# Kernel tuning notes

Measured on AMD Instinct MI355X. Metric: run time of the kernel, lower is better.

## Reference

```python
import jax, jax.numpy as jnp
import numpy as np

K_DIM, V_DIM, D_K, D_V, N_HEAD = 1024, 1024, 64, 64, 16


def setup_inputs() -> dict:
    key = jax.random.key(0)
    ks = jax.random.split(key, 7)
    B, LQ, LK = 2, 2048, 2048
    q = jax.random.normal(ks[0], (B, LQ, K_DIM), dtype=jnp.float32)
    k = jax.random.normal(ks[1], (B, LK, K_DIM), dtype=jnp.float32)
    v = jax.random.normal(ks[2], (B, LK, V_DIM), dtype=jnp.float32)
    s = 0.02
    w_q = jax.random.normal(ks[3], (N_HEAD * D_K, K_DIM), dtype=jnp.float32) * s
    w_k = jax.random.normal(ks[4], (N_HEAD * D_K, K_DIM), dtype=jnp.float32) * s
    w_v = jax.random.normal(ks[5], (N_HEAD * D_V, V_DIM), dtype=jnp.float32) * s
    fc_y = jax.random.normal(ks[6], (V_DIM, N_HEAD * D_V), dtype=jnp.float32) * s
    return {"q": q, "k": k, "v": v, "w_q": w_q, "w_k": w_k, "w_v": w_v, "fc_y": fc_y}


def reference(q, k, v, w_q, w_k, w_v, fc_y):
    B, LQ, _ = q.shape
    LK = k.shape[1]
    # projections: Linear(x) = x @ W.T, then split heads -> (b, h, l, d)
    qh = (q @ w_q.T).reshape(B, LQ, N_HEAD, D_K).transpose(0, 2, 1, 3)
    kh = (k @ w_k.T).reshape(B, LK, N_HEAD, D_K).transpose(0, 2, 1, 3)
    vh = (v @ w_v.T).reshape(B, LK, N_HEAD, D_V).transpose(0, 2, 1, 3)
    # NOTE: original ScaledDotProductAttention uses k.size(2), which for
    # 4D (b, h, len_k, d_k) inputs is len_k, NOT d_k. Replicate faithfully.
    scale = kh.shape[2] ** 0.5  # == sqrt(len_k)
    scores = jnp.einsum('bhqd,bhkd->bhqk', qh, kh) / scale
    attn = jax.nn.softmax(scores, axis=-1)  # (b, h, lq, lk)
    yh = jnp.einsum('bhqk,bhkd->bhqd', attn, vh)
    y = yh.transpose(0, 2, 1, 3).reshape(B, LQ, N_HEAD * D_V)
    y = y @ fc_y.T  # (b, lq, v_dim)
    return (y, attn)
```

## Files before the change

### kernel.cpp

```cpp
#include <hip/hip_runtime.h>

typedef __attribute__((ext_vector_type(8))) short short8;
typedef __attribute__((ext_vector_type(4))) short short4v;
typedef __attribute__((ext_vector_type(4))) float f32x4;

__device__ __forceinline__ short f2bf(float f) {
  unsigned u = __float_as_uint(f);
  u += 0x7fff + ((u >> 16) & 1);
  return (short)(u >> 16);
}

__device__ __forceinline__ void async16(const short* g, short* l) {
  __builtin_amdgcn_global_load_lds(
      (__attribute__((address_space(1))) unsigned int*)(g),
      (__attribute__((address_space(3))) unsigned int*)(l), 16, 0, 0);
}

__global__ __launch_bounds__(256) void cvt_w(const float* __restrict__ w0, const float* __restrict__ w1,
                                             const float* __restrict__ w2, const float* __restrict__ w3,
                                             short* __restrict__ o0, short* __restrict__ o1,
                                             short* __restrict__ o2, short* __restrict__ o3) {
  const int bid = blockIdx.x;
  const int seg = bid >> 9;
  const float* s = seg == 0 ? w0 : seg == 1 ? w1 : seg == 2 ? w2 : w3;
  short* d = seg == 0 ? o0 : seg == 1 ? o1 : seg == 2 ? o2 : o3;
  const int idx = ((bid & 511) * 256 + (int)threadIdx.x) * 8;
  float4 x = *(const float4*)(s + idx);
  float4 y = *(const float4*)(s + idx + 4);
  short8 t;
  t[0] = f2bf(x.x); t[1] = f2bf(x.y); t[2] = f2bf(x.z); t[3] = f2bf(x.w);
  t[4] = f2bf(y.x); t[5] = f2bf(y.y); t[6] = f2bf(y.z); t[7] = f2bf(y.w);
  *(short8*)(d + idx) = t;
}

__device__ __forceinline__ void ldf32(const float* src, int K, int kt, int tid, f32x4* r) {
  const int row = tid >> 4, c = (tid & 15) * 4;
  const float* p = src + (long)row * K + kt + c;
#pragma unroll
  for (int j = 0; j < 8; j++) r[j] = *(const f32x4*)(p + (long)(j * 16) * K);
}
__device__ __forceinline__ void wrf32(short* dst, int stride, int tid, const f32x4* r) {
  const int row = tid >> 4, c = (tid & 15) * 4;
#pragma unroll
  for (int j = 0; j < 8; j++) {
    short4v t;
    t[0] = f2bf(r[j][0]); t[1] = f2bf(r[j][1]); t[2] = f2bf(r[j][2]); t[3] = f2bf(r[j][3]);
    *(short4v*)&dst[(row + j * 16) * stride + c] = t;
  }
}
__device__ __forceinline__ void ldbf16(const short* src, int K, int kt, int tid, short* lds) {
  const int w = tid >> 6, l = tid & 63;
#pragma unroll
  for (int i = 0; i < 4; i++) {
    const int seg = i * 4 + w;
    const int o = seg * 1024 + l * 16;
    const int row = o >> 7, col = (o & 127) >> 1;
    async16(src + (long)row * K + kt + col, lds + seg * 512);
  }
}

template <int AF32, int BF32, int MODE>
__device__ __forceinline__ void gemm_core(const void* Ap, const void* Bp, void* Cout,
                                          int bm, int bn, int bz, int N, int K, int tid,
                                          short* As, short* Bs) {
  constexpr int SA = AF32 ? 72 : 64;
  constexpr int SB = BF32 ? 72 : 64;
  const int wave = tid >> 6, lane = tid & 63, quad = lane >> 4, l16 = lane & 15;
  const int wm = (wave >> 1) * 64, wn = (wave & 1) * 64;
  const float* A32 = (const float*)Ap + (long)bm * 128 * K;
  const short* A16 = (const short*)Ap + (long)bm * 128 * K;
  const float* B32 = (const float*)Bp + (long)bn * 128 * K;
  const short* B16 = (const short*)Bp + (long)bn * 128 * K;

  const f32x4 zero = {0.f, 0.f, 0.f, 0.f};
  f32x4 acc[4][4];
#pragma unroll
  for (int i = 0; i < 4; i++)
#pragma unroll
    for (int j = 0; j < 4; j++) acc[i][j] = zero;

  f32x4 ar[8], br[8];
  if (AF32) { ldf32(A32, K, 0, tid, ar); wrf32(As, SA, tid, ar); }
  else ldbf16(A16, K, 0, tid, As);
  if (BF32) { ldf32(B32, K, 0, tid, br); wrf32(Bs, SB, tid, br); }
  else ldbf16(B16, K, 0, tid, Bs);
  __syncthreads();

  const int NT = K >> 6;
  int cur = 0;
  for (int t = 0; t < NT; ++t) {
    short* Ac = As + cur * 128 * SA;
    short* Bc = Bs + cur * 128 * SB;
    short* An = As + (cur ^ 1) * 128 * SA;
    short* Bn = Bs + (cur ^ 1) * 128 * SB;
    const bool more = (t + 1 < NT);
    if (more) {
      if (AF32) ldf32(A32, K, (t + 1) * 64, tid, ar);
      else ldbf16(A16, K, (t + 1) * 64, tid, An);
      if (BF32) ldf32(B32, K, (t + 1) * 64, tid, br);
      else ldbf16(B16, K, (t + 1) * 64, tid, Bn);
    }
#pragma unroll
    for (int kk = 0; kk < 64; kk += 32) {
      short8 af[4], bf[4];
#pragma unroll
      for (int i = 0; i < 4; i++) af[i] = *(const short8*)&Ac[(wm + i * 16 + l16) * SA + kk + quad * 8];
#pragma unroll
      for (int j = 0; j < 4; j++) bf[j] = *(const short8*)&Bc[(wn + j * 16 + l16) * SB + kk + quad * 8];
#pragma unroll
      for (int i = 0; i < 4; i++)
#pragma unroll
        for (int j = 0; j < 4; j++)
          acc[i][j] = __builtin_amdgcn_mfma_f32_16x16x32_bf16(af[i], bf[j], acc[i][j], 0, 0, 0);
    }
    if (more) {
      if (AF32) wrf32(An, SA, tid, ar);
      if (BF32) wrf32(Bn, SB, tid, br);
    }
    __syncthreads();
    cur ^= 1;
  }

#pragma unroll
  for (int i = 0; i < 4; i++)
#pragma unroll
    for (int j = 0; j < 4; j++)
#pragma unroll
      for (int r = 0; r < 4; r++) {
        const int grow = bm * 128 + wm + i * 16 + quad * 4 + r;
        const int gcol = bn * 128 + wn + j * 16 + l16;
        const float val = acc[i][j][r];
        if (MODE == 0) {
          const int b = grow >> 11, l = grow & 2047, hh = gcol >> 6, d = gcol & 63;
          ((short*)Cout)[((long)(b * 16 + hh) * 2048 + l) * 64 + d] = f2bf(val);
        } else if (MODE == 1) {
          ((short*)Cout)[((long)bz * 1024 + grow) * 2048 + gcol] = f2bf(val);
        } else {
          ((float*)Cout)[(long)grow * N + gcol] = val;
        }
      }
}

__global__ __launch_bounds__(256) void proj_fused(const float* __restrict__ q, const float* __restrict__ k,
                                                  const float* __restrict__ v,
                                                  const short* __restrict__ wqb, const short* __restrict__ wkb,
                                                  const short* __restrict__ wvb,
                                                  short* __restrict__ qh, short* __restrict__ kh,
                                                  short* __restrict__ vht) {
  __shared__ __align__(16) short As[2 * 128 * 72];
  __shared__ __align__(16) short Bs[2 * 128 * 72];
  const int p = blockIdx.x, tid = threadIdx.x;
  const int id = (p & 7) * 96 + (p >> 3);
  if (id < 512) {
    const int seg = id >> 8, t = id & 255;
    const int bm = t >> 3, bn = t & 7;
    gemm_core<1, 0, 0>(seg ? (const void*)k : (const void*)q,
                       seg ? (const void*)wkb : (const void*)wqb,
                       seg ? (void*)kh : (void*)qh,
                       bm, bn, 0, 1024, 1024, tid, As, Bs);
  } else {
    const int lid = id - 512;
    const int bz = lid >> 7, t = lid & 127;
    gemm_core<0, 1, 1>(wvb, v + (long)bz * 2048 * 1024, vht,
                       t & 7, t >> 3, bz, 2048, 1024, tid, As, Bs);
  }
}

__global__ __launch_bounds__(256) void gemm_final(const short* __restrict__ yhb, const short* __restrict__ fcb,
                                                  float* __restrict__ y) {
  __shared__ __align__(16) short As[2 * 128 * 72];
  __shared__ __align__(16) short Bs[2 * 128 * 72];
  const int p = blockIdx.x;
  const int id = (p & 7) * 32 + (p >> 3);
  gemm_core<0, 0, 2>(yhb, fcb, y, id >> 3, id & 7, 0, 1024, 1024, threadIdx.x, As, Bs);
}

__global__ __launch_bounds__(256) void attn_kernel(const short* __restrict__ qh, const short* __restrict__ kh,
                                                   const short* __restrict__ vht,
                                                   float* __restrict__ attn_out, short* __restrict__ yhb) {
  __shared__ __align__(16) short k_s[64][72];
  __shared__ __align__(16) short v_s[64][72];
  __shared__ __align__(16) short p_s[64][72];
  constexpr float SCALE = 0.022097086912079608f;

  const int qb = blockIdx.x, h = blockIdx.y, b = blockIdx.z;
  const long bh = b * 16 + h;
  const short* Q = qh + bh * (2048L * 64) + (long)qb * 64 * 64;
  const short* Kp = kh + bh * (2048L * 64);
  const short* Vt = vht + bh * (64L * 2048);
  float* attnp = attn_out + bh * (2048L * 2048) + (long)qb * 64 * 2048;

  const int tid = threadIdx.x;
  const int wave = tid >> 6, lane = tid & 63, quad = lane >> 4, l16 = lane & 15;
  const int myrow0 = wave * 16;
  const int srow = tid >> 2, sch = (tid & 3) * 16;
  const f32x4 zero = {0.f, 0.f, 0.f, 0.f};

  const short8 qa0 = *(const short8*)(Q + (myrow0 + l16) * 64 + quad * 8);
  const short8 qa1 = *(const short8*)(Q + (myrow0 + l16) * 64 + 32 + quad * 8);

  float lrow[4] = {0.f, 0.f, 0.f, 0.f};
  f32x4 oacc[4];
#pragma unroll
  for (int nt = 0; nt < 4; ++nt) oacc[nt] = zero;

  *(short8*)&k_s[srow][sch] = *(const short8*)(Kp + srow * 64 + sch);
  *(short8*)&k_s[srow][sch + 8] = *(const short8*)(Kp + srow * 64 + sch + 8);
  *(short8*)&v_s[srow][sch] = *(const short8*)(Vt + (long)srow * 2048 + sch);
  *(short8*)&v_s[srow][sch + 8] = *(const short8*)(Vt + (long)srow * 2048 + sch + 8);
  __syncthreads();
  for (int kt = 0; kt < 32; ++kt) {
    short8 nk0, nk1, nv0, nv1;
    if (kt < 31) {
      const short* Kn = Kp + ((kt + 1) * 64 + srow) * 64 + sch;
      nk0 = *(const short8*)(Kn);
      nk1 = *(const short8*)(Kn + 8);
      const short* Vn = Vt + (long)srow * 2048 + (kt + 1) * 64 + sch;
      nv0 = *(const short8*)(Vn);
      nv1 = *(const short8*)(Vn + 8);
    }
#pragma unroll
    for (int nt = 0; nt < 4; ++nt) {
      short8 b0 = *(const short8*)&k_s[nt * 16 + l16][quad * 8];
      short8 b1 = *(const short8*)&k_s[nt * 16 + l16][32 + quad * 8];
      f32x4 c = zero;
      c = __builtin_amdgcn_mfma_f32_16x16x32_bf16(qa0, b0, c, 0, 0, 0);
      c = __builtin_amdgcn_mfma_f32_16x16x32_bf16(qa1, b1, c, 0, 0, 0);
#pragma unroll
      for (int r = 0; r < 4; ++r) {
        const float p = __expf(c[r] * SCALE);
        lrow[r] += p;
        p_s[myrow0 + quad * 4 + r][nt * 16 + l16] = f2bf(p);
      }
    }
    short8 pa0 = *(const short8*)&p_s[myrow0 + l16][quad * 8];
    short8 pa1 = *(const short8*)&p_s[myrow0 + l16][32 + quad * 8];
#pragma unroll
    for (int nt = 0; nt < 4; ++nt) {
      short8 vb0 = *(const short8*)&v_s[nt * 16 + l16][quad * 8];
      short8 vb1 = *(const short8*)&v_s[nt * 16 + l16][32 + quad * 8];
      oacc[nt] = __builtin_amdgcn_mfma_f32_16x16x32_bf16(pa0, vb0, oacc[nt], 0, 0, 0);
      oacc[nt] = __builtin_amdgcn_mfma_f32_16x16x32_bf16(pa1, vb1, oacc[nt], 0, 0, 0);
    }
    __syncthreads();
    if (kt < 31) {
      *(short8*)&k_s[srow][sch] = nk0;
      *(short8*)&k_s[srow][sch + 8] = nk1;
      *(short8*)&v_s[srow][sch] = nv0;
      *(short8*)&v_s[srow][sch + 8] = nv1;
    }
    __syncthreads();
  }

  float rinv[4];
#pragma unroll
  for (int r = 0; r < 4; ++r) {
    float l = lrow[r];
#pragma unroll
    for (int off = 1; off < 16; off <<= 1) l += __shfl_xor(l, off);
    rinv[r] = 1.0f / l;
  }

#pragma unroll
  for (int nt = 0; nt < 4; ++nt)
#pragma unroll
    for (int r = 0; r < 4; ++r) {
      const long l = (long)qb * 64 + myrow0 + quad * 4 + r;
      const int d = nt * 16 + l16;
      yhb[((long)b * 2048 + l) * 1024 + h * 64 + d] = f2bf(oacc[nt][r] * rinv[r]);
    }

  *(short8*)&k_s[srow][sch] = *(const short8*)(Kp + srow * 64 + sch);
  *(short8*)&k_s[srow][sch + 8] = *(const short8*)(Kp + srow * 64 + sch + 8);
  __syncthreads();
  for (int kt = 0; kt < 32; ++kt) {
    short(*cb)[72] = (kt & 1) ? v_s : k_s;
    short(*nb)[72] = (kt & 1) ? k_s : v_s;
    short8 n0, n1;
    if (kt < 31) {
      const short* Kn = Kp + ((kt + 1) * 64 + srow) * 64 + sch;
      n0 = *(const short8*)(Kn);
      n1 = *(const short8*)(Kn + 8);
    }
#pragma unroll
    for (int nt = 0; nt < 4; ++nt) {
      short8 b0 = *(const short8*)&cb[nt * 16 + l16][quad * 8];
      short8 b1 = *(const short8*)&cb[nt * 16 + l16][32 + quad * 8];
      f32x4 c = zero;
      c = __builtin_amdgcn_mfma_f32_16x16x32_bf16(qa0, b0, c, 0, 0, 0);
      c = __builtin_amdgcn_mfma_f32_16x16x32_bf16(qa1, b1, c, 0, 0, 0);
#pragma unroll
      for (int r = 0; r < 4; ++r) {
        const float pv = __expf(c[r] * SCALE) * rinv[r];
        __builtin_nontemporal_store(
            pv, &attnp[(long)(myrow0 + quad * 4 + r) * 2048 + kt * 64 + nt * 16 + l16]);
      }
    }
    if (kt < 31) {
      *(short8*)&nb[srow][sch] = n0;
      *(short8*)&nb[srow][sch + 8] = n1;
    }
    __syncthreads();
  }
}

extern "C" void kernel_launch(void* const* d_in, const int* in_sizes, int n_in,
                              void* d_out, int out_size, void* d_ws, size_t ws_size,
                              hipStream_t stream) {
  const float* q = (const float*)d_in[0];
  const float* k = (const float*)d_in[1];
  const float* v = (const float*)d_in[2];
  const float* wq = (const float*)d_in[3];
  const float* wk = (const float*)d_in[4];
  const float* wv = (const float*)d_in[5];
  const float* fcy = (const float*)d_in[6];

  float* y_out = (float*)d_out;
  float* attn_out = (float*)d_out + 4194304;

  char* ws = (char*)d_ws;
  short* qh = (short*)(ws);
  short* kh = (short*)(ws + 8388608);
  short* vht = (short*)(ws + 16777216);
  short* yhb = (short*)(ws + 25165824);
  short* wqb = (short*)(ws + 33554432);
  short* wkb = (short*)(ws + 35651584);
  short* wvb = (short*)(ws + 37748736);
  short* fcb = (short*)(ws + 39845888);

  cvt_w<<<2048, 256, 0, stream>>>(wq, wk, wv, fcy, wqb, wkb, wvb, fcb);
  proj_fused<<<768, 256, 0, stream>>>(q, k, v, wqb, wkb, wvb, qh, kh, vht);
  attn_kernel<<<dim3(32, 16, 2), 256, 0, stream>>>(qh, kh, vht, attn_out, yhb);
  gemm_final<<<dim3(256), 256, 0, stream>>>(yhb, fcb, y_out);
}
```

Baseline: 799.8 us.

## Pre-convert q/k/v activations to bf16 and split projections into bf16-only GEMMs

Adds conversion kernels that turn the fp32 q, k and v activations into bf16 scratch buffers, reusing workspace regions. The projection GEMMs then load only bf16 through async global-to-LDS copies. The GEMM core drops double buffering in favour of a single-buffered loop with two barriers per k-tile and smaller LDS, and launch bounds now request higher occupancy. The trade is extra passes over the activations and extra kernel launches, in exchange for cheaper GEMM inner loops and more resident blocks, with global latency hidden less by prefetching.

```diff
diff --git a/kernel.cpp b/kernel.cpp
--- a/kernel.cpp
+++ b/kernel.cpp
@@ -1,7 +1,6 @@
 #include <hip/hip_runtime.h>
 
 typedef __attribute__((ext_vector_type(8))) short short8;
-typedef __attribute__((ext_vector_type(4))) short short4v;
 typedef __attribute__((ext_vector_type(4))) float f32x4;
 
 __device__ __forceinline__ short f2bf(float f) {
@@ -16,38 +15,46 @@
       (__attribute__((address_space(3))) unsigned int*)(l), 16, 0, 0);
 }
 
-__global__ __launch_bounds__(256) void cvt_w(const float* __restrict__ w0, const float* __restrict__ w1,
-                                             const float* __restrict__ w2, const float* __restrict__ w3,
-                                             short* __restrict__ o0, short* __restrict__ o1,
-                                             short* __restrict__ o2, short* __restrict__ o3) {
+__global__ __launch_bounds__(256) void cvt1(
+    const float* __restrict__ w0, const float* __restrict__ w1,
+    const float* __restrict__ w2, const float* __restrict__ w3,
+    const float* __restrict__ qa, const float* __restrict__ ka,
+    short* __restrict__ ow0, short* __restrict__ ow1, short* __restrict__ ow2,
+    short* __restrict__ ow3, short* __restrict__ oq, short* __restrict__ ok) {
   const int bid = blockIdx.x;
-  const int seg = bid >> 9;
-  const float* s = seg == 0 ? w0 : seg == 1 ? w1 : seg == 2 ? w2 : w3;
-  short* d = seg == 0 ? o0 : seg == 1 ? o1 : seg == 2 ? o2 : o3;
-  const int idx = ((bid & 511) * 256 + (int)threadIdx.x) * 8;
-  float4 x = *(const float4*)(s + idx);
-  float4 y = *(const float4*)(s + idx + 4);
-  short8 t;
-  t[0] = f2bf(x.x); t[1] = f2bf(x.y); t[2] = f2bf(x.z); t[3] = f2bf(x.w);
-  t[4] = f2bf(y.x); t[5] = f2bf(y.y); t[6] = f2bf(y.z); t[7] = f2bf(y.w);
-  *(short8*)(d + idx) = t;
-}
-
-__device__ __forceinline__ void ldf32(const float* src, int K, int kt, int tid, f32x4* r) {
-  const int row = tid >> 4, c = (tid & 15) * 4;
-  const float* p = src + (long)row * K + kt + c;
-#pragma unroll
-  for (int j = 0; j < 8; j++) r[j] = *(const f32x4*)(p + (long)(j * 16) * K);
-}
-__device__ __forceinline__ void wrf32(short* dst, int stride, int tid, const f32x4* r) {
-  const int row = tid >> 4, c = (tid & 15) * 4;
-#pragma unroll
-  for (int j = 0; j < 8; j++) {
-    short4v t;
-    t[0] = f2bf(r[j][0]); t[1] = f2bf(r[j][1]); t[2] = f2bf(r[j][2]); t[3] = f2bf(r[j][3]);
-    *(short4v*)&dst[(row + j * 16) * stride + c] = t;
-  }
-}
+  const float* s;
+  short* d;
+  long idx;
+  if (bid < 2048) {
+    const int seg = bid >> 9;
+    s = seg == 0 ? w0 : seg == 1 ? w1 : seg == 2 ? w2 : w3;
+    d = seg == 0 ? ow0 : seg == 1 ? ow1 : seg == 2 ? ow2 : ow3;
+    idx = (long)(bid & 511) * 2048 + (long)threadIdx.x * 8;
+  } else {
+    const int t = bid - 2048;
+    const int seg = t >> 11;
+    s = seg == 0 ? qa : ka;
+    d = seg == 0 ? oq : ok;
+    idx = (long)(t & 2047) * 2048 + (long)threadIdx.x * 8;
+  }
+  const float4 x = *(const float4*)(s + idx);
+  const float4 y = *(const float4*)(s + idx + 4);
+  short8 t8;
+  t8[0] = f2bf(x.x); t8[1] = f2bf(x.y); t8[2] = f2bf(x.z); t8[3] = f2bf(x.w);
+  t8[4] = f2bf(y.x); t8[5] = f2bf(y.y); t8[6] = f2bf(y.z); t8[7] = f2bf(y.w);
+  *(short8*)(d + idx) = t8;
+}
+
+__global__ __launch_bounds__(256) void cvt2(const float* __restrict__ va, short* __restrict__ ov) {
+  const long idx = (long)blockIdx.x * 2048 + (long)threadIdx.x * 8;
+  const float4 x = *(const float4*)(va + idx);
+  const float4 y = *(const float4*)(va + idx + 4);
+  short8 t8;
+  t8[0] = f2bf(x.x); t8[1] = f2bf(x.y); t8[2] = f2bf(x.z); t8[3] = f2bf(x.w);
+  t8[4] = f2bf(y.x); t8[5] = f2bf(y.y); t8[6] = f2bf(y.z); t8[7] = f2bf(y.w);
+  *(short8*)(ov + idx) = t8;
+}
+
 __device__ __forceinline__ void ldbf16(const short* src, int K, int kt, int tid, short* lds) {
   const int w = tid >> 6, l = tid & 63;
 #pragma unroll
@@ -59,18 +66,14 @@
   }
 }
 
-template <int AF32, int BF32, int MODE>
-__device__ __forceinline__ void gemm_core(const void* Ap, const void* Bp, void* Cout,
-                                          int bm, int bn, int bz, int N, int K, int tid,
-                                          short* As, short* Bs) {
-  constexpr int SA = AF32 ? 72 : 64;
-  constexpr int SB = BF32 ? 72 : 64;
+template <int MODE>
+__device__ __forceinline__ void gemm_bf(const short* Aall, const short* Ball, void* Cout,
+                                        int bm, int bn, int bz, int N, int K, int tid,
+                                        short* As, short* Bs) {
   const int wave = tid >> 6, lane = tid & 63, quad = lane >> 4, l16 = lane & 15;
   const int wm = (wave >> 1) * 64, wn = (wave & 1) * 64;
-  const float* A32 = (const float*)Ap + (long)bm * 128 * K;
-  const short* A16 = (const short*)Ap + (long)bm * 128 * K;
-  const float* B32 = (const float*)Bp + (long)bn * 128 * K;
-  const short* B16 = (const short*)Bp + (long)bn * 128 * K;
+  const short* A = Aall + (long)bm * 128 * K;
+  const short* B = Ball + (long)bn * 128 * K;
 
   const f32x4 zero = {0.f, 0.f, 0.f, 0.f};
   f32x4 acc[4][4];
@@ -79,46 +82,24 @@
 #pragma unroll
     for (int j = 0; j < 4; j++) acc[i][j] = zero;
 
-  f32x4 ar[8], br[8];
-  if (AF32) { ldf32(A32, K, 0, tid, ar); wrf32(As, SA, tid, ar); }
-  else ldbf16(A16, K, 0, tid, As);
-  if (BF32) { ldf32(B32, K, 0, tid, br); wrf32(Bs, SB, tid, br); }
-  else ldbf16(B16, K, 0, tid, Bs);
-  __syncthreads();
-
-  const int NT = K >> 6;
-  int cur = 0;
-  for (int t = 0; t < NT; ++t) {
-    short* Ac = As + cur * 128 * SA;
-    short* Bc = Bs + cur * 128 * SB;
-    short* An = As + (cur ^ 1) * 128 * SA;
-    short* Bn = Bs + (cur ^ 1) * 128 * SB;
-    const bool more = (t + 1 < NT);
-    if (more) {
-      if (AF32) ldf32(A32, K, (t + 1) * 64, tid, ar);
-      else ldbf16(A16, K, (t + 1) * 64, tid, An);
-      if (BF32) ldf32(B32, K, (t + 1) * 64, tid, br);
-      else ldbf16(B16, K, (t + 1) * 64, tid, Bn);
-    }
+  for (int kt = 0; kt < K; kt += 64) {
+    __syncthreads();
+    ldbf16(A, K, kt, tid, As);
+    ldbf16(B, K, kt, tid, Bs);
+    __syncthreads();
 #pragma unroll
     for (int kk = 0; kk < 64; kk += 32) {
       short8 af[4], bf[4];
 #pragma unroll
-      for (int i = 0; i < 4; i++) af[i] = *(const short8*)&Ac[(wm + i * 16 + l16) * SA + kk + quad * 8];
-#pragma unroll
-      for (int j = 0; j < 4; j++) bf[j] = *(const short8*)&Bc[(wn + j * 16 + l16) * SB + kk + quad * 8];
+      for (int i = 0; i < 4; i++) af[i] = *(const short8*)&As[(wm + i * 16 + l16) * 64 + kk + quad * 8];
+#pragma unroll
+      for (int j = 0; j < 4; j++) bf[j] = *(const short8*)&Bs[(wn + j * 16 + l16) * 64 + kk + quad * 8];
 #pragma unroll
       for (int i = 0; i < 4; i++)
 #pragma unroll
         for (int j = 0; j < 4; j++)
           acc[i][j] = __builtin_amdgcn_mfma_f32_16x16x32_bf16(af[i], bf[j], acc[i][j], 0, 0, 0);
     }
-    if (more) {
-      if (AF32) wrf32(An, SA, tid, ar);
-      if (BF32) wrf32(Bn, SB, tid, br);
-    }
-    __syncthreads();
-    cur ^= 1;
   }
 
 #pragma unroll
@@ -141,43 +122,44 @@
       }
 }
 
-__global__ __launch_bounds__(256) void proj_fused(const float* __restrict__ q, const float* __restrict__ k,
-                                                  const float* __restrict__ v,
-                                                  const short* __restrict__ wqb, const short* __restrict__ wkb,
-                                                  const short* __restrict__ wvb,
-                                                  short* __restrict__ qh, short* __restrict__ kh,
-                                                  short* __restrict__ vht) {
-  __shared__ __align__(16) short As[2 * 128 * 72];
-  __shared__ __align__(16) short Bs[2 * 128 * 72];
+__global__ __launch_bounds__(256, 3) void proj_qk(
+    const short* __restrict__ qb, const short* __restrict__ kb,
+    const short* __restrict__ wqb, const short* __restrict__ wkb,
+    short* __restrict__ qh, short* __restrict__ kh) {
+  __shared__ __align__(16) short As[128 * 64];
+  __shared__ __align__(16) short Bs[128 * 64];
   const int p = blockIdx.x, tid = threadIdx.x;
-  const int id = (p & 7) * 96 + (p >> 3);
-  if (id < 512) {
-    const int seg = id >> 8, t = id & 255;
-    const int bm = t >> 3, bn = t & 7;
-    gemm_core<1, 0, 0>(seg ? (const void*)k : (const void*)q,
-                       seg ? (const void*)wkb : (const void*)wqb,
-                       seg ? (void*)kh : (void*)qh,
-                       bm, bn, 0, 1024, 1024, tid, As, Bs);
-  } else {
-    const int lid = id - 512;
-    const int bz = lid >> 7, t = lid & 127;
-    gemm_core<0, 1, 1>(wvb, v + (long)bz * 2048 * 1024, vht,
-                       t & 7, t >> 3, bz, 2048, 1024, tid, As, Bs);
-  }
-}
-
-__global__ __launch_bounds__(256) void gemm_final(const short* __restrict__ yhb, const short* __restrict__ fcb,
-                                                  float* __restrict__ y) {
-  __shared__ __align__(16) short As[2 * 128 * 72];
-  __shared__ __align__(16) short Bs[2 * 128 * 72];
+  const int id = (p & 7) * 64 + (p >> 3);
+  const int seg = id >> 8, t = id & 255;
+  gemm_bf<0>(seg ? kb : qb, seg ? wkb : wqb, seg ? (void*)kh : (void*)qh,
+             t >> 3, t & 7, 0, 1024, 1024, tid, As, Bs);
+}
+
+__global__ __launch_bounds__(256, 3) void proj_v(
+    const short* __restrict__ vb, const short* __restrict__ wvb, short* __restrict__ vht) {
+  __shared__ __align__(16) short As[128 * 64];
+  __shared__ __align__(16) short Bs[128 * 64];
+  const int p = blockIdx.x, tid = threadIdx.x;
+  const int id = (p & 7) * 32 + (p >> 3);
+  const int bz = id >> 7, t = id & 127;
+  gemm_bf<1>(wvb, vb + (long)bz * 2048 * 1024, vht, t & 7, t >> 3, bz, 2048, 1024, tid, As, Bs);
+}
+
+__global__ __launch_bounds__(256, 3) void gemm_final(const short* __restrict__ yhb,
+                                                     const short* __restrict__ fcb,
+                                                     float* __restrict__ y) {
+  __shared__ __align__(16) short As[128 * 64];
+  __shared__ __align__(16) short Bs[128 * 64];
   const int p = blockIdx.x;
   const int id = (p & 7) * 32 + (p >> 3);
-  gemm_core<0, 0, 2>(yhb, fcb, y, id >> 3, id & 7, 0, 1024, 1024, threadIdx.x, As, Bs);
-}
-
-__global__ __launch_bounds__(256) void attn_kernel(const short* __restrict__ qh, const short* __restrict__ kh,
-                                                   const short* __restrict__ vht,
-                                                   float* __restrict__ attn_out, short* __restrict__ yhb) {
+  gemm_bf<2>(yhb, fcb, y, id >> 3, id & 7, 0, 1024, 1024, threadIdx.x, As, Bs);
+}
+
+__global__ __launch_bounds__(256, 4) void attn_kernel(const short* __restrict__ qh,
+                                                      const short* __restrict__ kh,
+                                                      const short* __restrict__ vht,
+                                                      float* __restrict__ attn_out,
+                                                      short* __restrict__ yhb) {
   __shared__ __align__(16) short k_s[64][72];
   __shared__ __align__(16) short v_s[64][72];
   __shared__ __align__(16) short p_s[64][72];
@@ -319,17 +301,22 @@
   float* attn_out = (float*)d_out + 4194304;
 
   char* ws = (char*)d_ws;
-  short* qh = (short*)(ws);
-  short* kh = (short*)(ws + 8388608);
+  short* qh  = (short*)(ws);
+  short* kh  = (short*)(ws + 8388608);
   short* vht = (short*)(ws + 16777216);
   short* yhb = (short*)(ws + 25165824);
   short* wqb = (short*)(ws + 33554432);
   short* wkb = (short*)(ws + 35651584);
   short* wvb = (short*)(ws + 37748736);
   short* fcb = (short*)(ws + 39845888);
-
-  cvt_w<<<2048, 256, 0, stream>>>(wq, wk, wv, fcy, wqb, wkb, wvb, fcb);
-  proj_fused<<<768, 256, 0, stream>>>(q, k, v, wqb, wkb, wvb, qh, kh, vht);
+  short* qb16 = vht;
+  short* kb16 = yhb;
+  short* vb16 = yhb;
+
+  cvt1<<<6144, 256, 0, stream>>>(wq, wk, wv, fcy, q, k, wqb, wkb, wvb, fcb, qb16, kb16);
+  proj_qk<<<512, 256, 0, stream>>>(qb16, kb16, wqb, wkb, qh, kh);
+  cvt2<<<2048, 256, 0, stream>>>(v, vb16);
+  proj_v<<<256, 256, 0, stream>>>(vb16, wvb, vht);
   attn_kernel<<<dim3(32, 16, 2), 256, 0, stream>>>(qh, kh, vht, attn_out, yhb);
   gemm_final<<<dim3(256), 256, 0, stream>>>(yhb, fcb, y_out);
 }
```

Measured after the change: 764.1 us. 4.5% less time.
